# Kernel tuning notes

Hardware: AMD Instinct MI355X
Metric: run time of the kernel (lower is better)

Reference implementation:

```python
import jax, jax.numpy as jnp
import numpy as np

B, S, D, H, T = 64, 256, 256, 512, 48
EPS = 1e-5  # BatchNorm1d default eps


def setup_inputs():
    key = jax.random.key(0)
    ks = jax.random.split(key, 40)
    rn = lambda k, sh, s=0.05: jax.random.normal(k, sh, dtype=jnp.float32) * s
    inp = {}
    inp["inputs"] = jax.random.normal(ks[0], (B, S, D), dtype=jnp.float32)
    inp["tags"] = jax.random.randint(ks[1], (B, S), 0, T)
    i = 2
    for l, din in ((0, D), (1, 2 * H)):
        for d in ("f", "b"):
            inp["Wih_l%d%s" % (l, d)] = rn(ks[i], (4 * H, din)); i += 1
            inp["Whh_l%d%s" % (l, d)] = rn(ks[i], (4 * H, H)); i += 1
            inp["bih_l%d%s" % (l, d)] = rn(ks[i], (4 * H,)); i += 1
            inp["bhh_l%d%s" % (l, d)] = rn(ks[i], (4 * H,)); i += 1
    inp["bn_gamma"] = jnp.ones((2 * H,), jnp.float32)
    inp["bn_beta"] = jnp.zeros((2 * H,), jnp.float32)
    inp["bn_mean"] = rn(ks[i], (2 * H,)); i += 1
    inp["bn_var"] = jax.random.uniform(ks[i], (2 * H,), jnp.float32, 0.5, 1.5); i += 1
    inp["fc1_w"] = rn(ks[i], (H, 2 * H)); i += 1
    inp["fc1_b"] = rn(ks[i], (H,)); i += 1
    inp["fc2_w"] = rn(ks[i], (H // 2, H)); i += 1
    inp["fc2_b"] = rn(ks[i], (H // 2,)); i += 1
    inp["fc3_w"] = rn(ks[i], (T, H // 2)); i += 1
    inp["fc3_b"] = rn(ks[i], (T,)); i += 1
    inp["crf_start"] = rn(ks[i], (T,), 0.1); i += 1
    inp["crf_end"] = rn(ks[i], (T,), 0.1); i += 1
    inp["crf_trans"] = rn(ks[i], (T, T), 0.1); i += 1
    return inp


def _lstm_dir(x, Wih, Whh, bih, bhh, reverse):
    # x: [B,S,Din] -> hs: [B,S,H]; PyTorch gate order i,f,g,o
    xs = jnp.swapaxes(x, 0, 1)  # [S,B,Din]
    if reverse:
        xs = xs[::-1]
    pre = xs @ Wih.T + bih  # [S,B,4H] input projection precomputed
    h0 = jnp.zeros((x.shape[0], Whh.shape[1]), x.dtype)

    def step(carry, p):
        h, c = carry
        g = p + h @ Whh.T + bhh
        i, f, gg, o = jnp.split(g, 4, axis=-1)
        c = jax.nn.sigmoid(f) * c + jax.nn.sigmoid(i) * jnp.tanh(gg)
        h = jax.nn.sigmoid(o) * jnp.tanh(c)
        return (h, c), h

    _, hs = jax.lax.scan(step, (h0, h0), pre)
    if reverse:
        hs = hs[::-1]
    return jnp.swapaxes(hs, 0, 1)


def _model(inputs, tags, Wih_l0f, Whh_l0f, bih_l0f, bhh_l0f,
           Wih_l0b, Whh_l0b, bih_l0b, bhh_l0b,
           Wih_l1f, Whh_l1f, bih_l1f, bhh_l1f,
           Wih_l1b, Whh_l1b, bih_l1b, bhh_l1b,
           bn_gamma, bn_beta, bn_mean, bn_var,
           fc1_w, fc1_b, fc2_w, fc2_b, fc3_w, fc3_b,
           crf_start, crf_end, crf_trans):
    # 2-layer bidirectional LSTM
    x = jnp.concatenate([_lstm_dir(inputs, Wih_l0f, Whh_l0f, bih_l0f, bhh_l0f, False),
                         _lstm_dir(inputs, Wih_l0b, Whh_l0b, bih_l0b, bhh_l0b, True)], -1)
    x = jnp.concatenate([_lstm_dir(x, Wih_l1f, Whh_l1f, bih_l1f, bhh_l1f, False),
                         _lstm_dir(x, Wih_l1b, Whh_l1b, bih_l1b, bhh_l1b, True)], -1)
    # dropout: identity in eval; BatchNorm1d over channel dim, eval (running stats)
    x = (x - bn_mean) * (bn_gamma / jnp.sqrt(bn_var + EPS)) + bn_beta
    x = jax.nn.relu(x @ fc1_w.T + fc1_b)
    x = jax.nn.relu(x @ fc2_w.T + fc2_b)
    em = x @ fc3_w.T + fc3_b  # [B,S,T] emissions

    # CRF negative log-likelihood, full mask, reduction='mean'
    em_tag = jnp.take_along_axis(em, tags[..., None], axis=2)[..., 0]  # [B,S]
    num = (crf_start[tags[:, 0]] + em_tag.sum(1)
           + crf_trans[tags[:, :-1], tags[:, 1:]].sum(1)
           + crf_end[tags[:, -1]])

    et = jnp.swapaxes(em, 0, 1)  # [S,B,T]

    def step(alpha, e_t):
        # alpha: [B,T]; e_t: [B,T]
        alpha = jax.nn.logsumexp(alpha[:, :, None] + crf_trans[None], axis=1) + e_t
        return alpha, None

    alpha, _ = jax.lax.scan(step, crf_start + et[0], et[1:])
    logZ = jax.nn.logsumexp(alpha + crf_end, axis=1)
    return -jnp.mean(num - logZ)


def reference(inputs, tags, Wih_l0f, Whh_l0f, bih_l0f, bhh_l0f,
              Wih_l0b, Whh_l0b, bih_l0b, bhh_l0b,
              Wih_l1f, Whh_l1f, bih_l1f, bhh_l1f,
              Wih_l1b, Whh_l1b, bih_l1b, bhh_l1b,
              bn_gamma, bn_beta, bn_mean, bn_var,
              fc1_w, fc1_b, fc2_w, fc2_b, fc3_w, fc3_b,
              crf_start, crf_end, crf_trans):
    return _model(inputs, tags, Wih_l0f, Whh_l0f, bih_l0f, bhh_l0f,
                  Wih_l0b, Whh_l0b, bih_l0b, bhh_l0b,
                  Wih_l1f, Whh_l1f, bih_l1f, bhh_l1f,
                  Wih_l1b, Whh_l1b, bih_l1b, bhh_l1b,
                  bn_gamma, bn_beta, bn_mean, bn_var,
                  fc1_w, fc1_b, fc2_w, fc2_b, fc3_w, fc3_b,
                  crf_start, crf_end, crf_trans)
```

## Files before the change

kernel.cpp:

```cpp
#include <hip/hip_runtime.h>
#include <hip/hip_bf16.h>
#include <math.h>

#define Bz 64
#define Sz 256
#define Dz 256
#define Hz 512
#define FH 2048
#define OH 1024
#define Tz 48
#define EPSV 1e-5f
#define LOG2E 1.44269504f

typedef __hip_bfloat16 bf16;
typedef __attribute__((ext_vector_type(8))) short short8;
typedef __attribute__((ext_vector_type(4))) float floatx4;

__device__ __forceinline__ float b2f(bf16 v){ return __bfloat162float(v); }
__device__ __forceinline__ float fsig(float x){
  float e = __builtin_amdgcn_exp2f(-x*LOG2E);
  return __builtin_amdgcn_rcpf(1.f + e);
}
__device__ __forceinline__ float ftanh(float x){
  float e = __builtin_amdgcn_exp2f(x*(2.f*LOG2E));
  return 1.f - 2.f*__builtin_amdgcn_rcpf(e + 1.f);
}

__device__ __forceinline__ void load4f(const bf16* p, float v[4]) {
  ushort4 t = *(const ushort4*)p;
  v[0] = __uint_as_float(((unsigned)t.x) << 16);
  v[1] = __uint_as_float(((unsigned)t.y) << 16);
  v[2] = __uint_as_float(((unsigned)t.z) << 16);
  v[3] = __uint_as_float(((unsigned)t.w) << 16);
}
__device__ __forceinline__ void storev(float* p, float v){ *p = v; }
__device__ __forceinline__ void storev(bf16* p, float v){ *p = __float2bfloat16(v); }

__global__ __launch_bounds__(256) void castf2b(const float* __restrict__ in, bf16* __restrict__ out, int n)
{
  int i = (blockIdx.x*256 + threadIdx.x)*4;
  if (i >= n) return;
  float4 v = *(const float4*)(in + i);
  bf16 tmp[4];
  tmp[0] = __float2bfloat16(v.x); tmp[1] = __float2bfloat16(v.y);
  tmp[2] = __float2bfloat16(v.z); tmp[3] = __float2bfloat16(v.w);
  *(uint2*)(out + i) = *(const uint2*)tmp;
}

__global__ __launch_bounds__(256) void bnprep_k(const float* __restrict__ gamma, const float* __restrict__ beta,
  const float* __restrict__ mean, const float* __restrict__ var,
  float* __restrict__ scale, float* __restrict__ shift)
{
  int i = blockIdx.x*256 + threadIdx.x;
  if (i >= OH) return;
  float s = gamma[i]*rsqrtf(var[i]+EPSV);
  scale[i] = s; shift[i] = beta[i] - mean[i]*s;
}

template<typename TC>
__global__ __launch_bounds__(256) void gemm_mfma(
  const bf16* __restrict__ A, const bf16* __restrict__ W,
  const float* __restrict__ b1, const float* __restrict__ b2,
  TC* __restrict__ Cv, int M, int N, int K, int relu)
{
  __shared__ bf16 As[128][40];
  __shared__ bf16 Bs[128][40];
  int tid = threadIdx.x;
  int wave = tid>>6, lane = tid&63, l15 = lane&15, quad = lane>>4;
  int m0 = blockIdx.y*128, n0 = blockIdx.x*128;
  int wm = (wave>>1)*64, wn = (wave&1)*64;
  int srow = tid>>1, scw = (tid&1)*16;
  const bf16* Ap = A + (size_t)(m0+srow)*K + scw;
  const bf16* Wp = W + (size_t)(n0+srow)*K + scw;
  floatx4 zero = {0.f,0.f,0.f,0.f};
  floatx4 acc[4][4];
  #pragma unroll
  for (int i=0;i<4;i++)
    #pragma unroll
    for (int j=0;j<4;j++) acc[i][j] = zero;

  for (int k0 = 0; k0 < K; k0 += 32) {
    float4 a0 = *(const float4*)Ap, a1 = *(const float4*)(Ap+8);
    float4 w0 = *(const float4*)Wp, w1 = *(const float4*)(Wp+8);
    Ap += 32; Wp += 32;
    __syncthreads();
    *(float4*)&As[srow][scw]   = a0; *(float4*)&As[srow][scw+8] = a1;
    *(float4*)&Bs[srow][scw]   = w0; *(float4*)&Bs[srow][scw+8] = w1;
    __syncthreads();
    short8 af[4], bfv[4];
    #pragma unroll
    for (int mi=0;mi<4;mi++) af[mi]  = *(const short8*)&As[wm+mi*16+l15][quad*8];
    #pragma unroll
    for (int ni=0;ni<4;ni++) bfv[ni] = *(const short8*)&Bs[wn+ni*16+l15][quad*8];
    #pragma unroll
    for (int mi=0;mi<4;mi++)
      #pragma unroll
      for (int ni=0;ni<4;ni++)
        acc[mi][ni] = __builtin_amdgcn_mfma_f32_16x16x32_bf16(af[mi], bfv[ni], acc[mi][ni], 0,0,0);
  }
  #pragma unroll
  for (int mi=0;mi<4;mi++){
    #pragma unroll
    for (int ni=0;ni<4;ni++){
      int n = n0 + wn + ni*16 + l15;
      float bb = (b1 ? b1[n] : 0.f) + (b2 ? b2[n] : 0.f);
      #pragma unroll
      for (int r=0;r<4;r++){
        int m = m0 + wm + mi*16 + quad*4 + r;
        float v = acc[mi][ni][r] + bb;
        if (relu) v = fmaxf(v, 0.f);
        storev(&Cv[(size_t)m*N + n], v);
      }
    }
  }
}

__global__ __launch_bounds__(256) void gemm_nt_small(
  const bf16* __restrict__ A, const float* __restrict__ W,
  const float* __restrict__ b1, float* __restrict__ Cv, int M, int N, int K)
{
  __shared__ float As[8][128];
  __shared__ float Ws[8][128];
  int tid = threadIdx.x;
  int tx = tid & 15, ty = tid >> 4;
  int m0 = blockIdx.y * 128, n0 = blockIdx.x * 128;
  int sr = tid >> 1;
  int sk = (tid & 1) * 4;
  const bf16* Ap = A + (size_t)(m0 + sr) * K + sk;
  bool wok = (n0 + sr) < N;
  const float* Wp = W + (size_t)(wok ? (n0 + sr) : 0) * K + sk;
  float acc[8][8] = {};
  for (int k0 = 0; k0 < K; k0 += 8) {
    float av[4], wv[4];
    load4f(Ap, av);
    if (wok) { float4 t = *(const float4*)Wp; wv[0]=t.x; wv[1]=t.y; wv[2]=t.z; wv[3]=t.w; }
    else { wv[0]=wv[1]=wv[2]=wv[3]=0.f; }
    Ap += 8; Wp += 8;
    __syncthreads();
    As[sk+0][sr]=av[0]; As[sk+1][sr]=av[1]; As[sk+2][sr]=av[2]; As[sk+3][sr]=av[3];
    Ws[sk+0][sr]=wv[0]; Ws[sk+1][sr]=wv[1]; Ws[sk+2][sr]=wv[2]; Ws[sk+3][sr]=wv[3];
    __syncthreads();
    #pragma unroll
    for (int kk = 0; kk < 8; kk++) {
      float a[8], w[8];
      *(float4*)&a[0] = *(const float4*)&As[kk][ty*8];
      *(float4*)&a[4] = *(const float4*)&As[kk][ty*8+4];
      *(float4*)&w[0] = *(const float4*)&Ws[kk][tx*8];
      *(float4*)&w[4] = *(const float4*)&Ws[kk][tx*8+4];
      #pragma unroll
      for (int i=0;i<8;i++)
        #pragma unroll
        for (int j=0;j<8;j++) acc[i][j] += a[i]*w[j];
    }
  }
  #pragma unroll
  for (int i=0;i<8;i++){
    int m = m0 + ty*8 + i;
    #pragma unroll
    for (int j=0;j<8;j++){
      int n = n0 + tx*8 + j;
      if (n < N) Cv[(size_t)m*N + n] = acc[i][j] + b1[n];
    }
  }
}

__global__ __launch_bounds__(256,1) void lstm_persist(
  const bf16* __restrict__ preF, const bf16* __restrict__ preB,
  const bf16* __restrict__ WF, const bf16* __restrict__ WB,
  bf16* __restrict__ hbuf,
  bf16* __restrict__ xout,
  const float* __restrict__ bnscale, const float* __restrict__ bnshift,
  int* __restrict__ cnt)
{
  __shared__ bf16 wlds[64][520];
  int blk = blockIdx.x;
  int dir = blk & 1;
  int js  = blk >> 1;
  int j0  = js * 16;
  const bf16* pre = dir ? preB : preF;
  const bf16* W   = dir ? WB : WF;
  int colOff = dir ? Hz : 0;
  int tid = threadIdx.x;
  int wave = tid >> 6, lane = tid & 63, l15 = lane & 15, quad = lane >> 4;
  int* mycnt = cnt + dir*256;

  for (int chunk = tid; chunk < 64*64; chunk += 256) {
    int n = chunk >> 6, col = (chunk & 63) * 8;
    int g = n >> 4, idx = n & 15;
    *(float4*)&wlds[n][col] = *(const float4*)(W + ((size_t)(g*512 + j0 + idx))*Hz + col);
  }
  __syncthreads();

  int bb = wave*16 + quad*4;
  int j  = j0 + l15;
  float sc = bnscale ? bnscale[colOff + j] : 1.f;
  float sh = bnshift ? bnshift[colOff + j] : 0.f;
  int useBN = bnscale ? 1 : 0;
  float c[4] = {0.f,0.f,0.f,0.f};

  float pg[4][4];
  {
    int t0 = dir ? (Sz-1) : 0;
    #pragma unroll
    for (int r=0;r<4;r++){
      const bf16* pb = pre + ((size_t)(bb+r)*Sz + t0)*FH;
      #pragma unroll
      for (int g=0;g<4;g++) pg[g][r] = b2f(pb[g*512 + j]);
    }
  }

  for (int t = 0; t < Sz; t++) {
    int tcur = dir ? (Sz-1-t) : t;
    floatx4 zero = {0.f,0.f,0.f,0.f};
    floatx4 acc[4] = {zero, zero, zero, zero};

    short8 af[16];
    if (t > 0) {
      const bf16* hprev = hbuf + ((size_t)((t&1)*2 + dir))*Bz*Hz;
      #pragma unroll
      for (int ks=0;ks<16;ks++)
        af[ks] = *(const short8*)(hprev + (size_t)(wave*16 + l15)*Hz + ks*32 + quad*8);
    }

    float pgn[4][4];
    if (t+1 < Sz) {
      int tnext = dir ? (Sz-2-t) : (t+1);
      #pragma unroll
      for (int r=0;r<4;r++){
        const bf16* pb = pre + ((size_t)(bb+r)*Sz + tnext)*FH;
        #pragma unroll
        for (int g=0;g<4;g++) pgn[g][r] = b2f(pb[g*512 + j]);
      }
    }

    if (t > 0) {
      #pragma unroll
      for (int g=0; g<4; g++)
        #pragma unroll
        for (int ks=0; ks<16; ks++){
          short8 bfv = *(const short8*)&wlds[g*16 + l15][ks*32 + quad*8];
          acc[g] = __builtin_amdgcn_mfma_f32_16x16x32_bf16(af[ks], bfv, acc[g], 0,0,0);
        }
    }

    bf16* hnext = hbuf + ((size_t)(((t+1)&1)*2 + dir))*Bz*Hz;
    float hval[4];
    #pragma unroll
    for (int r=0;r<4;r++){
      int b = bb + r;
      float gi = acc[0][r] + pg[0][r];
      float gf = acc[1][r] + pg[1][r];
      float gg = acc[2][r] + pg[2][r];
      float go = acc[3][r] + pg[3][r];
      float cv = fsig(gf)*c[r] + fsig(gi)*ftanh(gg);
      float h  = fsig(go)*ftanh(cv);
      c[r] = cv;
      hval[r] = h;
      bf16 hb = __float2bfloat16(h);
      union { bf16 b16; short s; } u; u.b16 = hb;
      __hip_atomic_store((short*)(hnext + (size_t)b*Hz + j), u.s,
                         __ATOMIC_RELAXED, __HIP_MEMORY_SCOPE_AGENT);
    }

    if (t < Sz-1) {
      __syncthreads();
      if (tid == 0)
        __hip_atomic_fetch_add(&mycnt[t], 1, __ATOMIC_RELAXED, __HIP_MEMORY_SCOPE_AGENT);
    }

    #pragma unroll
    for (int r=0;r<4;r++){
      int b = bb + r;
      float xv = useBN ? (hval[r]*sc + sh) : hval[r];
      xout[((size_t)b*Sz + tcur)*OH + colOff + j] = __float2bfloat16(xv);
    }

    if (t < Sz-1) {
      if (tid == 0) {
        while (__hip_atomic_load(&mycnt[t], __ATOMIC_RELAXED, __HIP_MEMORY_SCOPE_AGENT) < 32) {}
      }
      __syncthreads();
      __builtin_amdgcn_fence(__ATOMIC_ACQUIRE, "agent");
    }

    if (t+1 < Sz) {
      #pragma unroll
      for (int g=0;g<4;g++)
        #pragma unroll
        for (int r=0;r<4;r++) pg[g][r] = pgn[g][r];
    }
  }
}

__global__ __launch_bounds__(64) void crf_k(const float* __restrict__ em, const int* __restrict__ tags,
  const float* __restrict__ start, const float* __restrict__ endv, const float* __restrict__ trans,
  float* __restrict__ result)
{
  __shared__ float tr[Tz*Tz];
  __shared__ float alpha[2][Tz];
  int b = blockIdx.x, tid = threadIdx.x;
  for (int i = tid; i < Tz*Tz; i += 64) tr[i] = trans[i];
  float np = 0.f;
  for (int t = tid; t < Sz; t += 64) {
    int tg = tags[b*Sz + t];
    np += em[((size_t)b*Sz + t)*Tz + tg];
    if (t+1 < Sz) np += trans[tg*Tz + tags[b*Sz + t + 1]];
  }
  #pragma unroll
  for (int off = 32; off; off >>= 1) np += __shfl_down(np, off);
  float num = 0.f;
  if (tid == 0) num = np + start[tags[b*Sz]] + endv[tags[b*Sz + Sz-1]];
  if (tid < Tz) alpha[0][tid] = start[tid] + em[((size_t)b*Sz)*Tz + tid];
  __syncthreads();
  int cur = 0;
  for (int t = 1; t < Sz; t++) {
    if (tid < Tz) {
      float m = -1e30f;
      for (int i = 0; i < Tz; i++) m = fmaxf(m, alpha[cur][i] + tr[i*Tz + tid]);
      float sum = 0.f;
      for (int i = 0; i < Tz; i++) sum += expf(alpha[cur][i] + tr[i*Tz + tid] - m);
      alpha[1-cur][tid] = m + logf(sum) + em[((size_t)b*Sz + t)*Tz + tid];
    }
    cur ^= 1;
    __syncthreads();
  }
  float a = (tid < Tz) ? alpha[cur][tid] + endv[tid] : -1e30f;
  float m = a;
  #pragma unroll
  for (int off = 32; off; off >>= 1) m = fmaxf(m, __shfl_down(m, off));
  m = __shfl(m, 0);
  float e = (tid < Tz) ? expf(a - m) : 0.f;
  #pragma unroll
  for (int off = 32; off; off >>= 1) e += __shfl_down(e, off);
  if (tid == 0) result[b] = num - (m + logf(e));
}

__global__ __launch_bounds__(64) void finalize_k(const float* __restrict__ result, float* __restrict__ outp)
{
  float v = result[threadIdx.x];
  #pragma unroll
  for (int off = 32; off; off >>= 1) v += __shfl_down(v, off);
  if (threadIdx.x == 0) outp[0] = -(v * (1.f/64.f));
}

extern "C" void kernel_launch(void* const* d_in, const int* in_sizes, int n_in,
                              void* d_out, int out_size, void* d_ws, size_t ws_size,
                              hipStream_t stream)
{
  (void)in_sizes; (void)n_in; (void)out_size; (void)ws_size;
  const float* inputs = (const float*)d_in[0];
  const int*   tags   = (const int*)d_in[1];
  const float* Wih[2][2] = {{(const float*)d_in[2],  (const float*)d_in[6]},
                            {(const float*)d_in[10], (const float*)d_in[14]}};
  const float* Whh[2][2] = {{(const float*)d_in[3],  (const float*)d_in[7]},
                            {(const float*)d_in[11], (const float*)d_in[15]}};
  const float* bih[2][2] = {{(const float*)d_in[4],  (const float*)d_in[8]},
                            {(const float*)d_in[12], (const float*)d_in[16]}};
  const float* bhh[2][2] = {{(const float*)d_in[5],  (const float*)d_in[9]},
                            {(const float*)d_in[13], (const float*)d_in[17]}};
  const float* bn_gamma = (const float*)d_in[18];
  const float* bn_beta  = (const float*)d_in[19];
  const float* bn_mean  = (const float*)d_in[20];
  const float* bn_var   = (const float*)d_in[21];
  const float* fc1_w = (const float*)d_in[22];
  const float* fc1_b = (const float*)d_in[23];
  const float* fc2_w = (const float*)d_in[24];
  const float* fc2_b = (const float*)d_in[25];
  const float* fc3_w = (const float*)d_in[26];
  const float* fc3_b = (const float*)d_in[27];
  const float* crf_start = (const float*)d_in[28];
  const float* crf_end   = (const float*)d_in[29];
  const float* crf_trans = (const float*)d_in[30];

  const size_t M = (size_t)Bz*Sz;
  char* p = (char*)d_ws;
  auto alloc = [&](size_t bytes) { char* r = p; p += (bytes + 255) & ~(size_t)255; return r; };
  bf16*  preF  = (bf16*) alloc(M*FH*sizeof(bf16));
  bf16*  preB  = (bf16*) alloc(M*FH*sizeof(bf16));
  bf16*  xbuf  = (bf16*) alloc(M*OH*sizeof(bf16));
  bf16*  inbf  = (bf16*) alloc(M*Dz*sizeof(bf16));
  bf16*  Wih0A = (bf16*) alloc((size_t)FH*Dz*sizeof(bf16));
  bf16*  Wih0B = (bf16*) alloc((size_t)FH*Dz*sizeof(bf16));
  bf16*  Wih1A = (bf16*) alloc((size_t)FH*OH*sizeof(bf16));
  bf16*  Wih1B = (bf16*) alloc((size_t)FH*OH*sizeof(bf16));
  bf16*  Whh0A = (bf16*) alloc((size_t)FH*Hz*sizeof(bf16));
  bf16*  Whh0B = (bf16*) alloc((size_t)FH*Hz*sizeof(bf16));
  bf16*  Whh1A = (bf16*) alloc((size_t)FH*Hz*sizeof(bf16));
  bf16*  Whh1B = (bf16*) alloc((size_t)FH*Hz*sizeof(bf16));
  bf16*  fc1wb = (bf16*) alloc((size_t)Hz*OH*sizeof(bf16));
  bf16*  fc2wb = (bf16*) alloc((size_t)256*Hz*sizeof(bf16));
  bf16*  hbuf  = (bf16*) alloc(4*(size_t)Bz*Hz*sizeof(bf16));
  int*   cnt   = (int*)  alloc(1024*sizeof(int));
  float* bnscale = (float*)alloc(OH*sizeof(float));
  float* bnshift = (float*)alloc(OH*sizeof(float));
  float* result  = (float*)alloc(Bz*sizeof(float));
  float* em   = (float*)inbf;
  bf16* fc1o = (bf16*)preF;
  bf16* fc2o = (bf16*)preB;

  dim3 tb(256);
  auto cast = [&](const float* src, bf16* dst, size_t n){
    castf2b<<<(n/4 + 255)/256, tb, 0, stream>>>(src, dst, (int)n);
  };

  hipMemsetAsync(cnt, 0, 1024*sizeof(int), stream);
  cast(inputs, inbf, M*Dz);
  cast(Wih[0][0], Wih0A, (size_t)FH*Dz);
  cast(Wih[0][1], Wih0B, (size_t)FH*Dz);
  cast(Wih[1][0], Wih1A, (size_t)FH*OH);
  cast(Wih[1][1], Wih1B, (size_t)FH*OH);
  cast(Whh[0][0], Whh0A, (size_t)FH*Hz);
  cast(Whh[0][1], Whh0B, (size_t)FH*Hz);
  cast(Whh[1][0], Whh1A, (size_t)FH*Hz);
  cast(Whh[1][1], Whh1B, (size_t)FH*Hz);
  cast(fc1_w, fc1wb, (size_t)Hz*OH);
  cast(fc2_w, fc2wb, (size_t)256*Hz);
  bnprep_k<<<OH/256, tb, 0, stream>>>(bn_gamma, bn_beta, bn_mean, bn_var, bnscale, bnshift);

  gemm_mfma<bf16><<<dim3(FH/128, M/128), tb, 0, stream>>>(inbf, Wih0A, bih[0][0], bhh[0][0], preF, M, FH, Dz, 0);
  gemm_mfma<bf16><<<dim3(FH/128, M/128), tb, 0, stream>>>(inbf, Wih0B, bih[0][1], bhh[0][1], preB, M, FH, Dz, 0);
  lstm_persist<<<64, tb, 0, stream>>>(preF, preB, Whh0A, Whh0B, hbuf, xbuf, nullptr, nullptr, cnt);
  gemm_mfma<bf16><<<dim3(FH/128, M/128), tb, 0, stream>>>(xbuf, Wih1A, bih[1][0], bhh[1][0], preF, M, FH, OH, 0);
  gemm_mfma<bf16><<<dim3(FH/128, M/128), tb, 0, stream>>>(xbuf, Wih1B, bih[1][1], bhh[1][1], preB, M, FH, OH, 0);
  lstm_persist<<<64, tb, 0, stream>>>(preF, preB, Whh1A, Whh1B, hbuf, xbuf, bnscale, bnshift, cnt + 512);
  gemm_mfma<bf16><<<dim3(Hz/128, M/128), tb, 0, stream>>>(xbuf, fc1wb, fc1_b, nullptr, fc1o, M, Hz, OH, 1);
  gemm_mfma<bf16><<<dim3(256/128, M/128), tb, 0, stream>>>(fc1o, fc2wb, fc2_b, nullptr, fc2o, M, 256, Hz, 1);
  gemm_nt_small<<<dim3(1, M/128), tb, 0, stream>>>(fc2o, fc3_w, fc3_b, em, M, Tz, 256);
  crf_k<<<Bz, 64, 0, stream>>>(em, tags, crf_start, crf_end, crf_trans, result);
  finalize_k<<<1, 64, 0, stream>>>(result, (float*)d_out);
}
```

Baseline: 4.549 ms.

## Replace block counter barrier with per-wave step flags polled by every wave

The grid-wide step barrier in the persistent LSTM kernel changes from a per-step atomic counter with __syncthreads plus single-thread spinning to per-wave monotonic flags. Each wave publishes its step number after its h stores drain, and all waves poll the 128 flags of their direction, which removes the intra-block syncthreads and atomic RMW from the critical path. The next-step pre-activation loads and xout stores are moved between the flag publish and the wait so they overlap the barrier latency. The cost is more polling traffic, since every wave reads 128 flags per step.

```diff
diff --git a/kernel.cpp b/kernel.cpp
--- a/kernel.cpp
+++ b/kernel.cpp
@@ -170,7 +170,7 @@
   bf16* __restrict__ hbuf,
   bf16* __restrict__ xout,
   const float* __restrict__ bnscale, const float* __restrict__ bnshift,
-  int* __restrict__ cnt)
+  int* __restrict__ flags)
 {
   __shared__ bf16 wlds[64][520];
   int blk = blockIdx.x;
@@ -182,7 +182,7 @@
   int colOff = dir ? Hz : 0;
   int tid = threadIdx.x;
   int wave = tid >> 6, lane = tid & 63, l15 = lane & 15, quad = lane >> 4;
-  int* mycnt = cnt + dir*256;
+  int* fl = flags + dir*128;
 
   for (int chunk = tid; chunk < 64*64; chunk += 256) {
     int n = chunk >> 6, col = (chunk & 63) * 8;
@@ -214,26 +214,12 @@
     floatx4 zero = {0.f,0.f,0.f,0.f};
     floatx4 acc[4] = {zero, zero, zero, zero};
 
-    short8 af[16];
     if (t > 0) {
       const bf16* hprev = hbuf + ((size_t)((t&1)*2 + dir))*Bz*Hz;
+      short8 af[16];
       #pragma unroll
       for (int ks=0;ks<16;ks++)
         af[ks] = *(const short8*)(hprev + (size_t)(wave*16 + l15)*Hz + ks*32 + quad*8);
-    }
-
-    float pgn[4][4];
-    if (t+1 < Sz) {
-      int tnext = dir ? (Sz-2-t) : (t+1);
-      #pragma unroll
-      for (int r=0;r<4;r++){
-        const bf16* pb = pre + ((size_t)(bb+r)*Sz + tnext)*FH;
-        #pragma unroll
-        for (int g=0;g<4;g++) pgn[g][r] = b2f(pb[g*512 + j]);
-      }
-    }
-
-    if (t > 0) {
       #pragma unroll
       for (int g=0; g<4; g++)
         #pragma unroll
@@ -263,31 +249,40 @@
     }
 
     if (t < Sz-1) {
-      __syncthreads();
-      if (tid == 0)
-        __hip_atomic_fetch_add(&mycnt[t], 1, __ATOMIC_RELAXED, __HIP_MEMORY_SCOPE_AGENT);
-    }
-
-    #pragma unroll
-    for (int r=0;r<4;r++){
-      int b = bb + r;
-      float xv = useBN ? (hval[r]*sc + sh) : hval[r];
-      xout[((size_t)b*Sz + tcur)*OH + colOff + j] = __float2bfloat16(xv);
-    }
-
-    if (t < Sz-1) {
-      if (tid == 0) {
-        while (__hip_atomic_load(&mycnt[t], __ATOMIC_RELAXED, __HIP_MEMORY_SCOPE_AGENT) < 32) {}
+      asm volatile("s_waitcnt vmcnt(0) lgkmcnt(0)" ::: "memory");
+      __hip_atomic_store(&fl[js*4 + wave], t+1, __ATOMIC_RELAXED, __HIP_MEMORY_SCOPE_AGENT);
+
+      int tnext = dir ? (Sz-2-t) : (t+1);
+      float pgn[4][4];
+      #pragma unroll
+      for (int r=0;r<4;r++){
+        const bf16* pb = pre + ((size_t)(bb+r)*Sz + tnext)*FH;
+        #pragma unroll
+        for (int g=0;g<4;g++) pgn[g][r] = b2f(pb[g*512 + j]);
       }
-      __syncthreads();
+      #pragma unroll
+      for (int r=0;r<4;r++){
+        float xv = useBN ? (hval[r]*sc + sh) : hval[r];
+        xout[((size_t)(bb+r)*Sz + tcur)*OH + colOff + j] = __float2bfloat16(xv);
+      }
+
+      int va, vb;
+      do {
+        va = __hip_atomic_load(&fl[lane],      __ATOMIC_RELAXED, __HIP_MEMORY_SCOPE_AGENT);
+        vb = __hip_atomic_load(&fl[64 + lane], __ATOMIC_RELAXED, __HIP_MEMORY_SCOPE_AGENT);
+      } while (__any(va <= t) | __any(vb <= t));
       __builtin_amdgcn_fence(__ATOMIC_ACQUIRE, "agent");
-    }
-
-    if (t+1 < Sz) {
+
       #pragma unroll
       for (int g=0;g<4;g++)
         #pragma unroll
         for (int r=0;r<4;r++) pg[g][r] = pgn[g][r];
+    } else {
+      #pragma unroll
+      for (int r=0;r<4;r++){
+        float xv = useBN ? (hval[r]*sc + sh) : hval[r];
+        xout[((size_t)(bb+r)*Sz + tcur)*OH + colOff + j] = __float2bfloat16(xv);
+      }
     }
   }
 }
@@ -390,7 +385,7 @@
   bf16*  fc1wb = (bf16*) alloc((size_t)Hz*OH*sizeof(bf16));
   bf16*  fc2wb = (bf16*) alloc((size_t)256*Hz*sizeof(bf16));
   bf16*  hbuf  = (bf16*) alloc(4*(size_t)Bz*Hz*sizeof(bf16));
-  int*   cnt   = (int*)  alloc(1024*sizeof(int));
+  int*   flags = (int*)  alloc(512*sizeof(int));
   float* bnscale = (float*)alloc(OH*sizeof(float));
   float* bnshift = (float*)alloc(OH*sizeof(float));
   float* result  = (float*)alloc(Bz*sizeof(float));
@@ -403,7 +398,7 @@
     castf2b<<<(n/4 + 255)/256, tb, 0, stream>>>(src, dst, (int)n);
   };
 
-  hipMemsetAsync(cnt, 0, 1024*sizeof(int), stream);
+  hipMemsetAsync(flags, 0, 512*sizeof(int), stream);
   cast(inputs, inbf, M*Dz);
   cast(Wih[0][0], Wih0A, (size_t)FH*Dz);
   cast(Wih[0][1], Wih0B, (size_t)FH*Dz);
@@ -419,10 +414,10 @@
 
   gemm_mfma<bf16><<<dim3(FH/128, M/128), tb, 0, stream>>>(inbf, Wih0A, bih[0][0], bhh[0][0], preF, M, FH, Dz, 0);
   gemm_mfma<bf16><<<dim3(FH/128, M/128), tb, 0, stream>>>(inbf, Wih0B, bih[0][1], bhh[0][1], preB, M, FH, Dz, 0);
-  lstm_persist<<<64, tb, 0, stream>>>(preF, preB, Whh0A, Whh0B, hbuf, xbuf, nullptr, nullptr, cnt);
+  lstm_persist<<<64, tb, 0, stream>>>(preF, preB, Whh0A, Whh0B, hbuf, xbuf, nullptr, nullptr, flags);
   gemm_mfma<bf16><<<dim3(FH/128, M/128), tb, 0, stream>>>(xbuf, Wih1A, bih[1][0], bhh[1][0], preF, M, FH, OH, 0);
   gemm_mfma<bf16><<<dim3(FH/128, M/128), tb, 0, stream>>>(xbuf, Wih1B, bih[1][1], bhh[1][1], preB, M, FH, OH, 0);
-  lstm_persist<<<64, tb, 0, stream>>>(preF, preB, Whh1A, Whh1B, hbuf, xbuf, bnscale, bnshift, cnt + 512);
+  lstm_persist<<<64, tb, 0, stream>>>(preF, preB, Whh1A, Whh1B, hbuf, xbuf, bnscale, bnshift, flags + 256);
   gemm_mfma<bf16><<<dim3(Hz/128, M/128), tb, 0, stream>>>(xbuf, fc1wb, fc1_b, nullptr, fc1o, M, Hz, OH, 1);
   gemm_mfma<bf16><<<dim3(256/128, M/128), tb, 0, stream>>>(fc1o, fc2wb, fc2_b, nullptr, fc2o, M, 256, Hz, 1);
   gemm_nt_small<<<dim3(1, M/128), tb, 0, stream>>>(fc2o, fc3_w, fc3_b, em, M, Tz, 256);
```

After: 5.463 ms. +20.1%, slower.
